# Kernel optimization log

Measured on AMD Instinct MI355X. Metric: run time of the kernel, lower is better.

## Reference

```python
import jax, jax.numpy as jnp
import numpy as np

D_MODEL = 768
NUM_HEADS = 12
HEAD_DIM = D_MODEL // NUM_HEADS  # 64, also rotary dim
INTERMEDIATE = 1152
WINDOW = 128          # config.local_attention (layer_id=1 -> local layer)
ROPE_BASE = 10000.0   # local_rope_theta
EPS = 1e-5


def layer_norm_nocenter(x, gamma):
    # keras LayerNormalization(center=False): mean-subtract, no beta
    mu = jnp.mean(x, axis=-1, keepdims=True)
    var = jnp.var(x, axis=-1, keepdims=True)
    return (x - mu) * jax.lax.rsqrt(var + EPS) * gamma


def rotate_half(x):
    x1, x2 = jnp.split(x, 2, axis=-1)
    return jnp.concatenate([-x2, x1], axis=-1)


def setup_inputs() -> dict:
    key = jax.random.key(0)
    ks = jax.random.split(key, 7)
    B, S = 4, 2048
    hidden_states = jax.random.normal(ks[0], (B, S, D_MODEL), dtype=jnp.float32)
    attention_mask = jnp.zeros((B, 1, S, S), dtype=jnp.float32)  # no padding
    s = 0.02
    attn_norm_gamma = jnp.ones((D_MODEL,), dtype=jnp.float32)
    wqkv = jax.random.normal(ks[1], (D_MODEL, 3 * D_MODEL), dtype=jnp.float32) * s
    wo_attn = jax.random.normal(ks[2], (D_MODEL, D_MODEL), dtype=jnp.float32) * s
    mlp_norm_gamma = jnp.ones((D_MODEL,), dtype=jnp.float32)
    wi = jax.random.normal(ks[3], (D_MODEL, 2 * INTERMEDIATE), dtype=jnp.float32) * s
    wo_mlp = jax.random.normal(ks[4], (INTERMEDIATE, D_MODEL), dtype=jnp.float32) * s
    return {
        'hidden_states': hidden_states,
        'attention_mask': attention_mask,
        'attn_norm_gamma': attn_norm_gamma,
        'wqkv': wqkv,
        'wo_attn': wo_attn,
        'mlp_norm_gamma': mlp_norm_gamma,
        'wi': wi,
        'wo_mlp': wo_mlp,
    }


def reference(hidden_states, attention_mask, attn_norm_gamma, wqkv, wo_attn,
              mlp_norm_gamma, wi, wo_mlp):
    B, S, Dm = hidden_states.shape
    H, Dh = NUM_HEADS, HEAD_DIM

    # RoPE cache (NTKScaling with scaling_factor=1 -> plain RoPE)
    idx = jnp.arange(0, Dh, 2, dtype=jnp.float32)
    inv_freq = 1.0 / (ROPE_BASE ** (idx / Dh))          # [Dh/2]
    t = jnp.arange(S, dtype=jnp.float32)
    freqs = t[:, None] * inv_freq[None, :]              # [S, Dh/2]
    emb = jnp.concatenate([freqs, freqs], axis=-1)      # [S, Dh]
    cos = jnp.cos(emb)[None, None]                      # [1,1,S,Dh]
    sin = jnp.sin(emb)[None, None]

    # combined sliding-window + padding mask
    pos = jnp.arange(S)
    dist = jnp.abs(pos[:, None] - pos[None, :])
    neg = jnp.finfo(jnp.float32).min
    local = jnp.where(dist <= WINDOW // 2, 0.0, neg).astype(jnp.float32)
    mask = attention_mask + local[None, None]           # [B,1,S,S]

    # attention (layer_id != 0 -> pre-norm)
    x = layer_norm_nocenter(hidden_states, attn_norm_gamma)
    qkv = (x @ wqkv).reshape(B, S, 3, H, Dh).transpose(2, 0, 3, 1, 4)
    q, k, v = qkv[0], qkv[1], qkv[2]                    # [B,H,S,Dh]
    q = q * cos + rotate_half(q) * sin
    k = k * cos + rotate_half(k) * sin

    scale = 1.0 / jnp.sqrt(jnp.asarray(Dh, q.dtype))
    scores = jnp.einsum('bhqd,bhkd->bhqk', q, k) * scale + mask
    attn = jax.nn.softmax(scores, axis=-1)
    ctx = jnp.einsum('bhqk,bhkd->bhqd', attn, v)
    attn_out = ctx.transpose(0, 2, 1, 3).reshape(B, S, Dm) @ wo_attn

    h = hidden_states + attn_out

    # GLU MLP: Wi -> split -> gelu(x)*gate -> Wo, residual
    n = layer_norm_nocenter(h, mlp_norm_gamma)
    x_in, gate = jnp.split(n @ wi, 2, axis=-1)
    mlp = jax.nn.gelu(x_in, approximate=False) * gate
    return h + mlp @ wo_mlp
```

## Files before the change

### kernel.cpp

```cpp
#include <hip/hip_runtime.h>
#include <cstdint>
#include <cstddef>

typedef __bf16 bf16;
typedef float f32x4 __attribute__((ext_vector_type(4)));
typedef __bf16 bf16x8 __attribute__((ext_vector_type(8)));
typedef __bf16 bf16x4 __attribute__((ext_vector_type(4)));
typedef __bf16 bf16x2 __attribute__((ext_vector_type(2)));

#define MFMA16(a, b, c) __builtin_amdgcn_mfma_f32_16x16x32_bf16((a), (b), (c), 0, 0, 0)

__device__ __forceinline__ void gload_lds16(const void* g, void* l) {
  __builtin_amdgcn_global_load_lds((__attribute__((address_space(1))) void*)g,
                                   (__attribute__((address_space(3))) void*)l,
                                   16, 0, 0);
}

__global__ __launch_bounds__(256) void wconv_ln(const float* __restrict__ wqkv,
                                                const float* __restrict__ woa,
                                                const float* __restrict__ wi,
                                                const float* __restrict__ wom,
                                                bf16* __restrict__ wqkvT,
                                                bf16* __restrict__ woaT,
                                                bf16* __restrict__ wiT,
                                                bf16* __restrict__ womT,
                                                const float* __restrict__ X,
                                                const float* __restrict__ gamma,
                                                bf16* __restrict__ xnout) {
  __shared__ float tile[32][33];
  const int t = threadIdx.x;
  int id = blockIdx.x;
  if (id >= 4896) {
    const int row = id - 4896;
    const float* xr = X + (size_t)row * 768;
    float v0 = xr[t], v1 = xr[t + 256], v2 = xr[t + 512];
    float s = v0 + v1 + v2;
    float s2 = v0 * v0 + v1 * v1 + v2 * v2;
#pragma unroll
    for (int m = 1; m <= 32; m <<= 1) {
      s += __shfl_xor(s, m, 64);
      s2 += __shfl_xor(s2, m, 64);
    }
    float* red = &tile[0][0];
    const int w = t >> 6, lane = t & 63;
    if (lane == 0) { red[w] = s; red[4 + w] = s2; }
    __syncthreads();
    s = red[0] + red[1] + red[2] + red[3];
    s2 = red[4] + red[5] + red[6] + red[7];
    const float mu = s * (1.f / 768.f);
    const float var = s2 * (1.f / 768.f) - mu * mu;
    const float rs = rsqrtf(var + 1e-5f);
    xnout[(size_t)row * 768 + t] = (bf16)((v0 - mu) * rs * gamma[t]);
    xnout[(size_t)row * 768 + t + 256] = (bf16)((v1 - mu) * rs * gamma[t + 256]);
    xnout[(size_t)row * 768 + t + 512] = (bf16)((v2 - mu) * rs * gamma[t + 512]);
    return;
  }
  const float* W;
  bf16* Wt;
  int K, N, bx, by;
  if (id < 1728) { W = wqkv; Wt = wqkvT; K = 768; N = 2304; bx = id % 72; by = id / 72; }
  else if (id < 2304) { id -= 1728; W = woa; Wt = woaT; K = 768; N = 768; bx = id % 24; by = id / 24; }
  else if (id < 4032) { id -= 2304; W = wi; Wt = wiT; K = 768; N = 2304; bx = id % 72; by = id / 72; }
  else { id -= 4032; W = wom; Wt = womT; K = 1152; N = 768; bx = id % 24; by = id / 24; }
  const int n0 = bx * 32, k0 = by * 32;
  const int c = t & 31, r = t >> 5;
#pragma unroll
  for (int i = 0; i < 4; ++i)
    tile[r + i * 8][c] = W[(size_t)(k0 + r + i * 8) * N + n0 + c];
  __syncthreads();
#pragma unroll
  for (int i = 0; i < 4; ++i)
    Wt[(size_t)(n0 + r + i * 8) * K + k0 + c] = (bf16)tile[c][r + i * 8];
}

__global__ __launch_bounds__(256) void ln_kernel(const float* __restrict__ X,
                                                 const float* __restrict__ gamma,
                                                 bf16* __restrict__ out) {
  const int row = blockIdx.x, t = threadIdx.x;
  const float* xr = X + (size_t)row * 768;
  float v0 = xr[t], v1 = xr[t + 256], v2 = xr[t + 512];
  float s = v0 + v1 + v2;
  float s2 = v0 * v0 + v1 * v1 + v2 * v2;
#pragma unroll
  for (int m = 1; m <= 32; m <<= 1) {
    s += __shfl_xor(s, m, 64);
    s2 += __shfl_xor(s2, m, 64);
  }
  __shared__ float red[8];
  const int w = t >> 6, lane = t & 63;
  if (lane == 0) { red[w] = s; red[4 + w] = s2; }
  __syncthreads();
  s = red[0] + red[1] + red[2] + red[3];
  s2 = red[4] + red[5] + red[6] + red[7];
  const float mu = s * (1.f / 768.f);
  const float var = s2 * (1.f / 768.f) - mu * mu;
  const float rs = rsqrtf(var + 1e-5f);
  out[(size_t)row * 768 + t] = (bf16)((v0 - mu) * rs * gamma[t]);
  out[(size_t)row * 768 + t + 256] = (bf16)((v1 - mu) * rs * gamma[t + 256]);
  out[(size_t)row * 768 + t + 512] = (bf16)((v2 - mu) * rs * gamma[t + 512]);
}

#define GEMM_CORE_LOOP(NT_, AROW_EXPR, BROW_EXPR)                                   \
  auto stage = [&](int tile) {                                                      \
    const int kk0 = tile * 64;                                                      \
    bf16* Ab_ = &SM[(tile & 1) * 24576];                                            \
    bf16* Bb_ = Ab_ + 16384;                                                        \
    _Pragma("unroll") for (int i = 0; i < 4; ++i) {                                 \
      int c = i * 512 + t;                                                          \
      int r = c >> 3, j = (c & 7) ^ (r & 7);                                        \
      gload_lds16(Ap + (size_t)(AROW_EXPR) * Kd + (kk0 + j * 8), &Ab_[c * 8]);      \
    }                                                                               \
    _Pragma("unroll") for (int i = 0; i < 2; ++i) {                                 \
      int c = i * 512 + t;                                                          \
      int r = c >> 3, j = (c & 7) ^ (r & 7);                                        \
      gload_lds16(Bp + (size_t)(BROW_EXPR) * Kd + (kk0 + j * 8), &Bb_[c * 8]);      \
    }                                                                               \
  };                                                                                \
  stage(0);                                                                         \
  stage(1);                                                                         \
  asm volatile("s_waitcnt vmcnt(6)" ::: "memory");                                  \
  __builtin_amdgcn_s_barrier();                                                     \
  __builtin_amdgcn_sched_barrier(0);                                                \
  for (int tt = 0; tt < NT_; ++tt) {                                                \
    const bf16* Ab = &SM[(tt & 1) * 24576];                                         \
    const bf16* Bb = Ab + 16384;                                                    \
    bf16x8 af[4], bfr[4];                                                           \
                                                                \
    _Pragma("unroll") for (int mt = 0; mt < 4; ++mt) {                              \
      int r = wm * 64 + mt * 16 + rm;                                               \
      af[mt] = *(const bf16x8*)&Ab[r * 64 + ((qd ^ (r & 7)) * 8)];                  \
    }                                                                               \
    _Pragma("unroll") for (int nt = 0; nt < 4; ++nt) {                              \
      int r = wn * 64 + nt * 16 + rm;                                               \
      bfr[nt] = *(const bf16x8*)&Bb[r * 64 + ((qd ^ (r & 7)) * 8)];                 \
    }                                                                               \
    __builtin_amdgcn_s_barrier();                                                   \
    __builtin_amdgcn_sched_barrier(0);                                              \
    __builtin_amdgcn_s_setprio(1);                                                  \
    _Pragma("unroll") for (int mt = 0; mt < 4; ++mt)                                \
        _Pragma("unroll") for (int nt = 0; nt < 4; ++nt)                            \
            acc[mt][nt] = MFMA16(af[mt], bfr[nt], acc[mt][nt]);                     \
    __builtin_amdgcn_s_setprio(0);                                                  \
    __builtin_amdgcn_s_barrier();                                                   \
    __builtin_amdgcn_sched_barrier(0);                                              \
                                                                \
    _Pragma("unroll") for (int mt = 0; mt < 4; ++mt) {                              \
      int r = wm * 64 + mt * 16 + rm;                                               \
      af[mt] = *(const bf16x8*)&Ab[r * 64 + (((4 + qd) ^ (r & 7)) * 8)];            \
    }                                                                               \
    _Pragma("unroll") for (int nt = 0; nt < 4; ++nt) {                              \
      int r = wn * 64 + nt * 16 + rm;                                               \
      bfr[nt] = *(const bf16x8*)&Bb[r * 64 + (((4 + qd) ^ (r & 7)) * 8)];           \
    }                                                                               \
    asm volatile("s_waitcnt lgkmcnt(0)" ::: "memory");                              \
    __builtin_amdgcn_sched_barrier(0);                                              \
    __builtin_amdgcn_s_barrier();           \
    __builtin_amdgcn_sched_barrier(0);                                              \
    if (tt + 2 < NT_) stage(tt + 2);                                                \
    __builtin_amdgcn_s_setprio(1);                                                  \
    _Pragma("unroll") for (int mt = 0; mt < 4; ++mt)                                \
        _Pragma("unroll") for (int nt = 0; nt < 4; ++nt)                            \
            acc[mt][nt] = MFMA16(af[mt], bfr[nt], acc[mt][nt]);                     \
    __builtin_amdgcn_s_setprio(0);                                                  \
    if (tt + 2 < NT_) {                                                             \
      asm volatile("s_waitcnt vmcnt(6)" ::: "memory");                              \
    } else {                                                                        \
      asm volatile("s_waitcnt vmcnt(0)" ::: "memory");                              \
    }                                                                               \
    __builtin_amdgcn_s_barrier();                                                   \
    __builtin_amdgcn_sched_barrier(0);                                              \
  }

template <int EPI, int NT>
__global__ __launch_bounds__(512, 2) void gemm_big(const bf16* __restrict__ Ap,
                                                   const bf16* __restrict__ Bp,
                                                   const float* __restrict__ Res,
                                                   void* __restrict__ Cout,
                                                   int Nout) {
  constexpr int Kd = NT * 64;
  __shared__ __align__(16) bf16 SM[49152];
  const int t = threadIdx.x;
  const int lane = t & 63, w = t >> 6;
  const int wm = w >> 1, wn = w & 1;
  const int rm = lane & 15, qd = lane >> 4;
  const int by = blockIdx.y;
  const int row0 = blockIdx.x * 256;
  f32x4 acc[4][4] = {};

  auto brow = [&](int r) -> int {
    if constexpr (EPI == 1) {
      int q = (r >> 4) & 3;
      return ((q & 1) ? 1152 : 0) + by * 64 + (r >> 6) * 32 + ((q >> 1) << 4) + (r & 15);
    } else {
      return by * 128 + r;
    }
  };

  GEMM_CORE_LOOP(NT, row0 + r, brow(r))

  if constexpr (EPI == 0) {
    float* C = (float*)Cout;
#pragma unroll
    for (int mt = 0; mt < 4; ++mt)
#pragma unroll
      for (int nt = 0; nt < 4; ++nt) {
        const int gc = by * 128 + wn * 64 + nt * 16 + rm;
#pragma unroll
        for (int r = 0; r < 4; ++r) {
          const int gr = row0 + wm * 64 + mt * 16 + qd * 4 + r;
          const size_t idx = (size_t)gr * Nout + gc;
          C[idx] = Res[idx] + acc[mt][nt][r];
        }
      }
  } else {
    bf16* C = (bf16*)Cout;
#pragma unroll
    for (int mt = 0; mt < 4; ++mt)
#pragma unroll
      for (int g = 0; g < 2; ++g) {
        const int gc = by * 64 + wn * 32 + g * 16 + rm;
#pragma unroll
        for (int r = 0; r < 4; ++r) {
          const int gr = row0 + wm * 64 + mt * 16 + qd * 4 + r;
          const float x = acc[mt][g * 2][r], gv = acc[mt][g * 2 + 1][r];
          const float ge = 0.5f * x * (1.0f + erff(x * 0.70710678118654752f));
          C[(size_t)gr * 1152 + gc] = (bf16)(ge * gv);
        }
      }
  }
}

__global__ __launch_bounds__(512, 2) void gemm_qkv2(const bf16* __restrict__ Ap,
                                                    const bf16* __restrict__ Bp,
                                                    bf16* __restrict__ Qb,
                                                    bf16* __restrict__ Kb,
                                                    bf16* __restrict__ Vt) {
  constexpr int Kd = 768;
  __shared__ __align__(16) bf16 SM[49152];
  const int t = threadIdx.x;
  const int lane = t & 63, w = t >> 6;
  const int wm = w >> 1, wn = w & 1;
  const int rm = lane & 15, qd = lane >> 4;
  const int by = blockIdx.y;
  const int row0 = blockIdx.x * 256;
  f32x4 acc[4][4] = {};

  GEMM_CORE_LOOP(12, row0 + r, by * 128 + r)

  const int head_id = by * 2 + wn;
  const int typ = by / 6;
  const int b = row0 >> 11;
  const int sblk = row0 & 2047;
  const int sw = sblk + wm * 64;

  if (typ < 2) {
    const int h = head_id - typ * 12;
    const size_t bhbase = (size_t)(b * 12 + h) * 2048;
    bf16* dst = typ ? Kb : Qb;
    constexpr float inv2pi = 0.15915494309189535f;
#pragma unroll
    for (int nt = 0; nt < 2; ++nt) {
      const int d = nt * 16 + rm;
      const float invf = exp2f((float)d * -0.41524101186092029f);
      float rev = (float)(sw + qd * 4) * invf * inv2pi;
      rev -= floorf(rev);
      float cs = __builtin_amdgcn_cosf(rev);
      float sn = __builtin_amdgcn_sinf(rev);
      float rv1 = invf * inv2pi;
      float c1 = __builtin_amdgcn_cosf(rv1), s1 = __builtin_amdgcn_sinf(rv1);
      float rv13 = 13.f * invf * inv2pi;
      rv13 -= floorf(rv13);
      float c13 = __builtin_amdgcn_cosf(rv13), s13 = __builtin_amdgcn_sinf(rv13);
#pragma unroll
      for (int mt = 0; mt < 4; ++mt)
#pragma unroll
        for (int r = 0; r < 4; ++r) {
          const int s = sw + mt * 16 + qd * 4 + r;
          const float x1 = acc[mt][nt][r], x2 = acc[mt][nt + 2][r];
          bf16x2 v2;
          v2[0] = (bf16)(x1 * cs - x2 * sn);
          v2[1] = (bf16)(x2 * cs + x1 * sn);
          *(bf16x2*)&dst[(bhbase + s) * 64 + 2 * d] = v2;
          const float ca = (r < 3) ? c1 : c13, sa = (r < 3) ? s1 : s13;
          const float cn = cs * ca - sn * sa;
          sn = sn * ca + cs * sa;
          cs = cn;
        }
    }
  } else {
#pragma unroll
    for (int mt = 0; mt < 4; ++mt)
#pragma unroll
      for (int nt = 0; nt < 4; ++nt) {
        int hd = wn * 64 + nt * 16 + rm;
        int sl = wm * 64 + mt * 16 + qd * 4;
        bf16x4 v4;
#pragma unroll
        for (int r = 0; r < 4; ++r) v4[r] = (bf16)acc[mt][nt][r];
        *(bf16x4*)&SM[hd * 264 + sl] = v4;
      }
    __syncthreads();
    const int h0 = by * 2 - 24;
#pragma unroll
    for (int it = 0; it < 8; ++it) {
      int cc = it * 512 + t;
      int hd = cc >> 5, s8 = (cc & 31) * 8;
      bf16x8 vv = *(const bf16x8*)&SM[hd * 264 + s8];
      size_t grow = (size_t)(b * 12 + h0 + (hd >> 6)) * 64 + (hd & 63);
      *(bf16x8*)&Vt[grow * 2048 + sblk + s8] = vv;
    }
  }
}

__global__ __launch_bounds__(256) void attn_kernel(const bf16* __restrict__ Qb,
                                                   const bf16* __restrict__ Kb,
                                                   const bf16* __restrict__ Vt,
                                                   const float* __restrict__ am,
                                                   bf16* __restrict__ ctx) {
  __shared__ __align__(16) bf16 KP[64 * 200];
  __shared__ __align__(16) bf16 Vts[64 * 192];
  bf16* Ks = KP;
  bf16* Ps = KP;

  const int t = threadIdx.x;
  const int lane = t & 63, w = t >> 6;
  const int rm = lane & 15, qd = lane >> 4;
  const int s0 = blockIdx.x * 64;
  const int bh = blockIdx.y;
  const int b = bh / 12, h = bh - b * 12;
  const size_t baseQ = (size_t)bh * 2048;

#pragma unroll
  for (int i = 0; i < 6; ++i) {
    int c = i * 256 + t;
    int r = c >> 3, j = (c & 7) ^ (r & 7);
    int key = min(max(s0 - 64 + r, 0), 2047);
    gload_lds16(Kb + (baseQ + key) * 64 + j * 8, &Ks[c * 8]);
  }
#pragma unroll
  for (int i = 0; i < 6; ++i) {
    int c = i * 256 + t;
    int r = c / 24, jl = c - r * 24;
    int j = (jl & 24) | ((jl & 7) ^ (r & 7));
    int k0 = min(max(s0 - 64 + j * 8, 0), 2040);
    gload_lds16(Vt + ((size_t)bh * 64 + r) * 2048 + k0, &Vts[c * 8]);
  }

  bf16x8 aq[2];
#pragma unroll
  for (int kb = 0; kb < 2; ++kb)
    aq[kb] = *(const bf16x8*)&Qb[(baseQ + s0 + w * 16 + rm) * 64 + kb * 32 + qd * 8];

  float msk[12][4];
#pragma unroll
  for (int nt = 0; nt < 12; ++nt) {
    int key = s0 - 64 + nt * 16 + rm;
#pragma unroll
    for (int r = 0; r < 4; ++r) {
      int qpos = s0 + w * 16 + qd * 4 + r;
      bool valid = (key >= 0) && (key < 2048) && (key - qpos <= 64) && (qpos - key <= 64);
      msk[nt][r] = valid ? am[((size_t)b * 2048 + qpos) * 2048 + key] : -3e38f;
    }
  }
  __syncthreads();

  f32x4 sc[12];
#pragma unroll
  for (int nt = 0; nt < 12; ++nt) {
    f32x4 a = {0.f, 0.f, 0.f, 0.f};
#pragma unroll
    for (int kb = 0; kb < 2; ++kb) {
      int r = nt * 16 + rm;
      bf16x8 bk = *(const bf16x8*)&Ks[r * 64 + (((kb * 4 + qd) ^ (rm & 7)) * 8)];
      a = MFMA16(aq[kb], bk, a);
    }
    sc[nt] = a;
  }

  float mx[4] = {-3e38f, -3e38f, -3e38f, -3e38f};
#pragma unroll
  for (int nt = 0; nt < 12; ++nt)
#pragma unroll
    for (int r = 0; r < 4; ++r) {
      float v = (msk[nt][r] <= -2.9e38f) ? -3e38f : sc[nt][r] * 0.125f + msk[nt][r];
      sc[nt][r] = v;
      mx[r] = fmaxf(mx[r], v);
    }
#pragma unroll
  for (int r = 0; r < 4; ++r)
#pragma unroll
    for (int m = 1; m <= 8; m <<= 1) mx[r] = fmaxf(mx[r], __shfl_xor(mx[r], m, 64));
  float sum[4] = {0.f, 0.f, 0.f, 0.f};
#pragma unroll
  for (int nt = 0; nt < 12; ++nt)
#pragma unroll
    for (int r = 0; r < 4; ++r) {
      float p = (sc[nt][r] > -1e37f) ? __expf(sc[nt][r] - mx[r]) : 0.f;
      sc[nt][r] = p;
      sum[r] += p;
    }
#pragma unroll
  for (int r = 0; r < 4; ++r)
#pragma unroll
    for (int m = 1; m <= 8; m <<= 1) sum[r] += __shfl_xor(sum[r], m, 64);
  float inv[4];
#pragma unroll
  for (int r = 0; r < 4; ++r) inv[r] = 1.f / sum[r];

  __syncthreads();

#pragma unroll
  for (int nt = 0; nt < 12; ++nt)
#pragma unroll
    for (int r = 0; r < 4; ++r)
      Ps[(w * 16 + qd * 4 + r) * 200 + nt * 16 + rm] = (bf16)(sc[nt][r] * inv[r]);

  f32x4 o[4] = {};
#pragma unroll
  for (int ks = 0; ks < 6; ++ks) {
    bf16x8 ap = *(const bf16x8*)&Ps[(w * 16 + rm) * 200 + ks * 32 + qd * 8];
#pragma unroll
    for (int nt = 0; nt < 4; ++nt) {
      int kc = ks * 4 + qd;
      bf16x8 bv = *(const bf16x8*)&Vts[(nt * 16 + rm) * 192 +
                                       (((kc & 24) | ((kc & 7) ^ (rm & 7))) * 8)];
      o[nt] = MFMA16(ap, bv, o[nt]);
    }
  }
#pragma unroll
  for (int nt = 0; nt < 4; ++nt)
#pragma unroll
    for (int r = 0; r < 4; ++r) {
      int q_ = s0 + w * 16 + qd * 4 + r;
      ctx[((size_t)(b * 2048 + q_)) * 768 + h * 64 + nt * 16 + rm] = (bf16)o[nt][r];
    }
}

extern "C" void kernel_launch(void* const* d_in, const int* in_sizes, int n_in,
                              void* d_out, int out_size, void* d_ws, size_t ws_size,
                              hipStream_t stream) {
  (void)in_sizes; (void)n_in; (void)out_size; (void)ws_size;
  const float* hidden = (const float*)d_in[0];
  const float* amask = (const float*)d_in[1];
  const float* g1 = (const float*)d_in[2];
  const float* wqkv = (const float*)d_in[3];
  const float* woa = (const float*)d_in[4];
  const float* g2 = (const float*)d_in[5];
  const float* wi = (const float*)d_in[6];
  const float* wom = (const float*)d_in[7];
  float* out = (float*)d_out;

  char* p = (char*)d_ws;
  size_t o = 0;
  auto take = [&](size_t bytes) {
    char* r = p + o;
    o = (o + bytes + 255) & ~(size_t)255;
    return r;
  };
  bf16* wqkvT = (bf16*)take((size_t)2304 * 768 * 2);
  bf16* woaT = (bf16*)take((size_t)768 * 768 * 2);
  bf16* wiT = (bf16*)take((size_t)2304 * 768 * 2);
  bf16* womT = (bf16*)take((size_t)768 * 1152 * 2);
  bf16* xn = (bf16*)take((size_t)8192 * 768 * 2);
  bf16* Qb = (bf16*)take((size_t)98304 * 64 * 2);
  bf16* Kb = (bf16*)take((size_t)98304 * 64 * 2);
  bf16* Vt = (bf16*)take((size_t)98304 * 64 * 2);
  bf16* ctxb = (bf16*)take((size_t)8192 * 768 * 2);
  float* hbuf = (float*)take((size_t)8192 * 768 * 4);
  bf16* mlp = (bf16*)take((size_t)8192 * 1152 * 2);

  wconv_ln<<<13088, 256, 0, stream>>>(wqkv, woa, wi, wom, wqkvT, woaT, wiT, womT,
                                      hidden, g1, xn);

  gemm_qkv2<<<dim3(32, 18), 512, 0, stream>>>(xn, wqkvT, Qb, Kb, Vt);
  attn_kernel<<<dim3(32, 48), 256, 0, stream>>>(Qb, Kb, Vt, amask, ctxb);
  gemm_big<0, 12><<<dim3(32, 6), 512, 0, stream>>>(ctxb, woaT, hidden, hbuf, 768);

  ln_kernel<<<8192, 256, 0, stream>>>(hbuf, g2, xn);
  gemm_big<1, 12><<<dim3(32, 18), 512, 0, stream>>>(xn, wiT, nullptr, mlp, 1152);
  gemm_big<0, 18><<<dim3(32, 6), 512, 0, stream>>>(mlp, womT, hbuf, out, 768);
}
```

Measured before the change: 307.8 us.

## Triple-buffer GEMM LDS tiles and collapse per-k-tile barriers to one

Switches the shared GEMM main loop from double to triple buffering of LDS tiles. The prefetch of tile tt+2 is now issued at the top of each iteration. Both half-k MFMA phases run back-to-back with a single barrier per iteration, replacing the four barriers and the setprio toggling. This is meant to cut barrier stalls and start global loads earlier. LDS per block grows from 96KB to 144KB, so the requested two blocks per CU likely no longer fit in LDS, which halves occupancy.

```diff
diff --git a/kernel.cpp b/kernel.cpp
--- a/kernel.cpp
+++ b/kernel.cpp
@@ -103,7 +103,7 @@
 #define GEMM_CORE_LOOP(NT_, AROW_EXPR, BROW_EXPR)                                   \
   auto stage = [&](int tile) {                                                      \
     const int kk0 = tile * 64;                                                      \
-    bf16* Ab_ = &SM[(tile & 1) * 24576];                                            \
+    bf16* Ab_ = &SM[(tile % 3) * 24576];                                            \
     bf16* Bb_ = Ab_ + 16384;                                                        \
     _Pragma("unroll") for (int i = 0; i < 4; ++i) {                                 \
       int c = i * 512 + t;                                                          \
@@ -122,51 +122,27 @@
   __builtin_amdgcn_s_barrier();                                                     \
   __builtin_amdgcn_sched_barrier(0);                                                \
   for (int tt = 0; tt < NT_; ++tt) {                                                \
-    const bf16* Ab = &SM[(tt & 1) * 24576];                                         \
+    if (tt + 2 < NT_) stage(tt + 2);                                                \
+    const bf16* Ab = &SM[(tt % 3) * 24576];                                         \
     const bf16* Bb = Ab + 16384;                                                    \
     bf16x8 af[4], bfr[4];                                                           \
-                                                                \
-    _Pragma("unroll") for (int mt = 0; mt < 4; ++mt) {                              \
-      int r = wm * 64 + mt * 16 + rm;                                               \
-      af[mt] = *(const bf16x8*)&Ab[r * 64 + ((qd ^ (r & 7)) * 8)];                  \
+    _Pragma("unroll") for (int kb = 0; kb < 2; ++kb) {                              \
+      _Pragma("unroll") for (int mt = 0; mt < 4; ++mt) {                            \
+        int r = wm * 64 + mt * 16 + rm;                                             \
+        af[mt] = *(const bf16x8*)&Ab[r * 64 + (((kb * 4 + qd) ^ (r & 7)) * 8)];     \
+      }                                                                             \
+      _Pragma("unroll") for (int nt = 0; nt < 4; ++nt) {                            \
+        int r = wn * 64 + nt * 16 + rm;                                             \
+        bfr[nt] = *(const bf16x8*)&Bb[r * 64 + (((kb * 4 + qd) ^ (r & 7)) * 8)];    \
+      }                                                                             \
+      _Pragma("unroll") for (int mt = 0; mt < 4; ++mt)                              \
+          _Pragma("unroll") for (int nt = 0; nt < 4; ++nt)                          \
+              acc[mt][nt] = MFMA16(af[mt], bfr[nt], acc[mt][nt]);                   \
     }                                                                               \
-    _Pragma("unroll") for (int nt = 0; nt < 4; ++nt) {                              \
-      int r = wn * 64 + nt * 16 + rm;                                               \
-      bfr[nt] = *(const bf16x8*)&Bb[r * 64 + ((qd ^ (r & 7)) * 8)];                 \
-    }                                                                               \
-    __builtin_amdgcn_s_barrier();                                                   \
     __builtin_amdgcn_sched_barrier(0);                                              \
-    __builtin_amdgcn_s_setprio(1);                                                  \
-    _Pragma("unroll") for (int mt = 0; mt < 4; ++mt)                                \
-        _Pragma("unroll") for (int nt = 0; nt < 4; ++nt)                            \
-            acc[mt][nt] = MFMA16(af[mt], bfr[nt], acc[mt][nt]);                     \
-    __builtin_amdgcn_s_setprio(0);                                                  \
-    __builtin_amdgcn_s_barrier();                                                   \
-    __builtin_amdgcn_sched_barrier(0);                                              \
-                                                                \
-    _Pragma("unroll") for (int mt = 0; mt < 4; ++mt) {                              \
-      int r = wm * 64 + mt * 16 + rm;                                               \
-      af[mt] = *(const bf16x8*)&Ab[r * 64 + (((4 + qd) ^ (r & 7)) * 8)];            \
-    }                                                                               \
-    _Pragma("unroll") for (int nt = 0; nt < 4; ++nt) {                              \
-      int r = wn * 64 + nt * 16 + rm;                                               \
-      bfr[nt] = *(const bf16x8*)&Bb[r * 64 + (((4 + qd) ^ (r & 7)) * 8)];           \
-    }                                                                               \
     asm volatile("s_waitcnt lgkmcnt(0)" ::: "memory");                              \
-    __builtin_amdgcn_sched_barrier(0);                                              \
-    __builtin_amdgcn_s_barrier();           \
-    __builtin_amdgcn_sched_barrier(0);                                              \
-    if (tt + 2 < NT_) stage(tt + 2);                                                \
-    __builtin_amdgcn_s_setprio(1);                                                  \
-    _Pragma("unroll") for (int mt = 0; mt < 4; ++mt)                                \
-        _Pragma("unroll") for (int nt = 0; nt < 4; ++nt)                            \
-            acc[mt][nt] = MFMA16(af[mt], bfr[nt], acc[mt][nt]);                     \
-    __builtin_amdgcn_s_setprio(0);                                                  \
-    if (tt + 2 < NT_) {                                                             \
-      asm volatile("s_waitcnt vmcnt(6)" ::: "memory");                              \
-    } else {                                                                        \
-      asm volatile("s_waitcnt vmcnt(0)" ::: "memory");                              \
-    }                                                                               \
+    if (tt + 2 < NT_) { asm volatile("s_waitcnt vmcnt(6)" ::: "memory"); }          \
+    else if (tt + 1 < NT_) { asm volatile("s_waitcnt vmcnt(0)" ::: "memory"); }     \
     __builtin_amdgcn_s_barrier();                                                   \
     __builtin_amdgcn_sched_barrier(0);                                              \
   }
@@ -178,7 +154,7 @@
                                                    void* __restrict__ Cout,
                                                    int Nout) {
   constexpr int Kd = NT * 64;
-  __shared__ __align__(16) bf16 SM[49152];
+  __shared__ __align__(16) bf16 SM[73728];
   const int t = threadIdx.x;
   const int lane = t & 63, w = t >> 6;
   const int wm = w >> 1, wn = w & 1;
@@ -236,7 +212,7 @@
                                                     bf16* __restrict__ Kb,
                                                     bf16* __restrict__ Vt) {
   constexpr int Kd = 768;
-  __shared__ __align__(16) bf16 SM[49152];
+  __shared__ __align__(16) bf16 SM[73728];
   const int t = threadIdx.x;
   const int lane = t & 63, w = t >> 6;
   const int wm = w >> 1, wn = w & 1;
```

Result: no change. 304.9 us (-0.9%).

## Enlarge GEMM tiles to 256x256 with BK=32 and 4-stage LDS pipeline

Applied to the files above, without the earlier changes.

The shared GEMM core loop now uses 256x256 output tiles per block, with 8 waves laid out 2x4 and 8x4 accumulator fragments per wave. K tiles shrink to 32 with a four-buffer LDS ring, and global-to-LDS loads for the next tile are interleaved between the two MFMA halves. The aim is more reuse per loaded byte and better hiding of load latency. The cost is that grids halve (e.g. 32x3 = 96 blocks for the output projections, below the CU count), accumulator register pressure doubles, and LDS use rises, which can hurt occupancy.

```diff
diff --git a/kernel.cpp b/kernel.cpp
--- a/kernel.cpp
+++ b/kernel.cpp
@@ -101,72 +101,64 @@
 }
 
 #define GEMM_CORE_LOOP(NT_, AROW_EXPR, BROW_EXPR)                                   \
-  auto stage = [&](int tile) {                                                      \
-    const int kk0 = tile * 64;                                                      \
-    bf16* Ab_ = &SM[(tile & 1) * 24576];                                            \
-    bf16* Bb_ = Ab_ + 16384;                                                        \
-    _Pragma("unroll") for (int i = 0; i < 4; ++i) {                                 \
-      int c = i * 512 + t;                                                          \
-      int r = c >> 3, j = (c & 7) ^ (r & 7);                                        \
+  auto stagep = [&](int tile, int p) {                                              \
+    const int kk0 = tile * 32;                                                      \
+    bf16* Ab_ = &SM[(tile & 3) * 16384];                                            \
+    bf16* Bb_ = Ab_ + 8192;                                                         \
+    {                                                                               \
+      int c = p * 512 + t;                                                          \
+      int r = c >> 2, j = (c & 3) ^ (r & 3);                                        \
       gload_lds16(Ap + (size_t)(AROW_EXPR) * Kd + (kk0 + j * 8), &Ab_[c * 8]);      \
     }                                                                               \
-    _Pragma("unroll") for (int i = 0; i < 2; ++i) {                                 \
-      int c = i * 512 + t;                                                          \
-      int r = c >> 3, j = (c & 7) ^ (r & 7);                                        \
+    {                                                                               \
+      int c = p * 512 + t;                                                          \
+      int r = c >> 2, j = (c & 3) ^ (r & 3);                                        \
       gload_lds16(Bp + (size_t)(BROW_EXPR) * Kd + (kk0 + j * 8), &Bb_[c * 8]);      \
     }                                                                               \
   };                                                                                \
-  stage(0);                                                                         \
-  stage(1);                                                                         \
-  asm volatile("s_waitcnt vmcnt(6)" ::: "memory");                                  \
+  stagep(0, 0); stagep(0, 1);                                                       \
+  stagep(1, 0); stagep(1, 1);                                                       \
+  asm volatile("s_waitcnt vmcnt(4)" ::: "memory");                                  \
   __builtin_amdgcn_s_barrier();                                                     \
   __builtin_amdgcn_sched_barrier(0);                                                \
   for (int tt = 0; tt < NT_; ++tt) {                                                \
-    const bf16* Ab = &SM[(tt & 1) * 24576];                                         \
-    const bf16* Bb = Ab + 16384;                                                    \
+    const bf16* Ab = &SM[(tt & 3) * 16384];                                         \
+    const bf16* Bb = Ab + 8192;                                                     \
     bf16x8 af[4], bfr[4];                                                           \
-                                                                \
-    _Pragma("unroll") for (int mt = 0; mt < 4; ++mt) {                              \
-      int r = wm * 64 + mt * 16 + rm;                                               \
-      af[mt] = *(const bf16x8*)&Ab[r * 64 + ((qd ^ (r & 7)) * 8)];                  \
-    }                                                                               \
+                       \
     _Pragma("unroll") for (int nt = 0; nt < 4; ++nt) {                              \
       int r = wn * 64 + nt * 16 + rm;                                               \
-      bfr[nt] = *(const bf16x8*)&Bb[r * 64 + ((qd ^ (r & 7)) * 8)];                 \
+      bfr[nt] = *(const bf16x8*)&Bb[r * 32 + ((qd ^ (r & 3)) * 8)];                 \
     }                                                                               \
+    _Pragma("unroll") for (int mt = 0; mt < 4; ++mt) {                              \
+      int r = wm * 128 + mt * 16 + rm;                                              \
+      af[mt] = *(const bf16x8*)&Ab[r * 32 + ((qd ^ (r & 3)) * 8)];                  \
+    }                                                                               \
+    if (tt + 2 < NT_) stagep(tt + 2, 0);                                            \
     __builtin_amdgcn_s_barrier();                                                   \
     __builtin_amdgcn_sched_barrier(0);                                              \
     __builtin_amdgcn_s_setprio(1);                                                  \
     _Pragma("unroll") for (int mt = 0; mt < 4; ++mt)                                \
-        _Pragma("unroll") for (int nt = 0; nt < 4; ++nt)                            \
-            acc[mt][nt] = MFMA16(af[mt], bfr[nt], acc[mt][nt]);                     \
+      _Pragma("unroll") for (int nt = 0; nt < 4; ++nt)                              \
+        acc[mt][nt] = MFMA16(af[mt], bfr[nt], acc[mt][nt]);                         \
     __builtin_amdgcn_s_setprio(0);                                                  \
     __builtin_amdgcn_s_barrier();                                                   \
     __builtin_amdgcn_sched_barrier(0);                                              \
-                                                                \
+                                                        \
     _Pragma("unroll") for (int mt = 0; mt < 4; ++mt) {                              \
-      int r = wm * 64 + mt * 16 + rm;                                               \
-      af[mt] = *(const bf16x8*)&Ab[r * 64 + (((4 + qd) ^ (r & 7)) * 8)];            \
+      int r = wm * 128 + 64 + mt * 16 + rm;                                         \
+      af[mt] = *(const bf16x8*)&Ab[r * 32 + ((qd ^ (r & 3)) * 8)];                  \
     }                                                                               \
-    _Pragma("unroll") for (int nt = 0; nt < 4; ++nt) {                              \
-      int r = wn * 64 + nt * 16 + rm;                                               \
-      bfr[nt] = *(const bf16x8*)&Bb[r * 64 + (((4 + qd) ^ (r & 7)) * 8)];           \
-    }                                                                               \
-    asm volatile("s_waitcnt lgkmcnt(0)" ::: "memory");                              \
+    if (tt + 2 < NT_) stagep(tt + 2, 1);                                            \
+    __builtin_amdgcn_s_barrier();                                                   \
     __builtin_amdgcn_sched_barrier(0);                                              \
-    __builtin_amdgcn_s_barrier();           \
-    __builtin_amdgcn_sched_barrier(0);                                              \
-    if (tt + 2 < NT_) stage(tt + 2);                                                \
     __builtin_amdgcn_s_setprio(1);                                                  \
     _Pragma("unroll") for (int mt = 0; mt < 4; ++mt)                                \
-        _Pragma("unroll") for (int nt = 0; nt < 4; ++nt)                            \
-            acc[mt][nt] = MFMA16(af[mt], bfr[nt], acc[mt][nt]);                     \
+      _Pragma("unroll") for (int nt = 0; nt < 4; ++nt)                              \
+        acc[4 + mt][nt] = MFMA16(af[mt], bfr[nt], acc[4 + mt][nt]);                 \
     __builtin_amdgcn_s_setprio(0);                                                  \
-    if (tt + 2 < NT_) {                                                             \
-      asm volatile("s_waitcnt vmcnt(6)" ::: "memory");                              \
-    } else {                                                                        \
-      asm volatile("s_waitcnt vmcnt(0)" ::: "memory");                              \
-    }                                                                               \
+    if (tt + 2 < NT_) { asm volatile("s_waitcnt vmcnt(4)" ::: "memory"); }          \
+    else { asm volatile("s_waitcnt vmcnt(0)" ::: "memory"); }                       \
     __builtin_amdgcn_s_barrier();                                                   \
     __builtin_amdgcn_sched_barrier(0);                                              \
   }
@@ -177,22 +169,23 @@
                                                    const float* __restrict__ Res,
                                                    void* __restrict__ Cout,
                                                    int Nout) {
-  constexpr int Kd = NT * 64;
-  __shared__ __align__(16) bf16 SM[49152];
+  constexpr int Kd = NT * 32;
+  __shared__ __align__(16) bf16 SM[65536];
   const int t = threadIdx.x;
   const int lane = t & 63, w = t >> 6;
-  const int wm = w >> 1, wn = w & 1;
+  const int wm = w >> 2, wn = w & 3;
   const int rm = lane & 15, qd = lane >> 4;
   const int by = blockIdx.y;
   const int row0 = blockIdx.x * 256;
-  f32x4 acc[4][4] = {};
+  f32x4 acc[8][4] = {};
 
   auto brow = [&](int r) -> int {
     if constexpr (EPI == 1) {
       int q = (r >> 4) & 3;
-      return ((q & 1) ? 1152 : 0) + by * 64 + (r >> 6) * 32 + ((q >> 1) << 4) + (r & 15);
+      return ((q & 1) ? 1152 : 0) + by * 128 + ((r >> 6) * 32) + (((q >> 1) & 1) * 16) +
+             (r & 15);
     } else {
-      return by * 128 + r;
+      return by * 256 + r;
     }
   };
 
@@ -201,13 +194,13 @@
   if constexpr (EPI == 0) {
     float* C = (float*)Cout;
 #pragma unroll
-    for (int mt = 0; mt < 4; ++mt)
+    for (int mt = 0; mt < 8; ++mt)
 #pragma unroll
       for (int nt = 0; nt < 4; ++nt) {
-        const int gc = by * 128 + wn * 64 + nt * 16 + rm;
+        const int gc = by * 256 + wn * 64 + nt * 16 + rm;
 #pragma unroll
         for (int r = 0; r < 4; ++r) {
-          const int gr = row0 + wm * 64 + mt * 16 + qd * 4 + r;
+          const int gr = row0 + wm * 128 + mt * 16 + qd * 4 + r;
           const size_t idx = (size_t)gr * Nout + gc;
           C[idx] = Res[idx] + acc[mt][nt][r];
         }
@@ -215,13 +208,13 @@
   } else {
     bf16* C = (bf16*)Cout;
 #pragma unroll
-    for (int mt = 0; mt < 4; ++mt)
+    for (int mt = 0; mt < 8; ++mt)
 #pragma unroll
       for (int g = 0; g < 2; ++g) {
-        const int gc = by * 64 + wn * 32 + g * 16 + rm;
+        const int gc = by * 128 + wn * 32 + g * 16 + rm;
 #pragma unroll
         for (int r = 0; r < 4; ++r) {
-          const int gr = row0 + wm * 64 + mt * 16 + qd * 4 + r;
+          const int gr = row0 + wm * 128 + mt * 16 + qd * 4 + r;
           const float x = acc[mt][g * 2][r], gv = acc[mt][g * 2 + 1][r];
           const float ge = 0.5f * x * (1.0f + erff(x * 0.70710678118654752f));
           C[(size_t)gr * 1152 + gc] = (bf16)(ge * gv);
@@ -236,25 +229,24 @@
                                                     bf16* __restrict__ Kb,
                                                     bf16* __restrict__ Vt) {
   constexpr int Kd = 768;
-  __shared__ __align__(16) bf16 SM[49152];
+  __shared__ __align__(16) bf16 SM[69632];
   const int t = threadIdx.x;
   const int lane = t & 63, w = t >> 6;
-  const int wm = w >> 1, wn = w & 1;
+  const int wm = w >> 2, wn = w & 3;
   const int rm = lane & 15, qd = lane >> 4;
   const int by = blockIdx.y;
   const int row0 = blockIdx.x * 256;
-  f32x4 acc[4][4] = {};
-
-  GEMM_CORE_LOOP(12, row0 + r, by * 128 + r)
-
-  const int head_id = by * 2 + wn;
-  const int typ = by / 6;
+  f32x4 acc[8][4] = {};
+
+  GEMM_CORE_LOOP(24, row0 + r, by * 256 + r)
+
+  const int typ = by / 3;
   const int b = row0 >> 11;
   const int sblk = row0 & 2047;
-  const int sw = sblk + wm * 64;
+  const int sw = sblk + wm * 128;
 
   if (typ < 2) {
-    const int h = head_id - typ * 12;
+    const int h = (by % 3) * 4 + wn;
     const size_t bhbase = (size_t)(b * 12 + h) * 2048;
     bf16* dst = typ ? Kb : Qb;
     constexpr float inv2pi = 0.15915494309189535f;
@@ -272,7 +264,7 @@
       rv13 -= floorf(rv13);
       float c13 = __builtin_amdgcn_cosf(rv13), s13 = __builtin_amdgcn_sinf(rv13);
 #pragma unroll
-      for (int mt = 0; mt < 4; ++mt)
+      for (int mt = 0; mt < 8; ++mt)
 #pragma unroll
         for (int r = 0; r < 4; ++r) {
           const int s = sw + mt * 16 + qd * 4 + r;
@@ -289,20 +281,20 @@
     }
   } else {
 #pragma unroll
-    for (int mt = 0; mt < 4; ++mt)
+    for (int mt = 0; mt < 8; ++mt)
 #pragma unroll
       for (int nt = 0; nt < 4; ++nt) {
         int hd = wn * 64 + nt * 16 + rm;
-        int sl = wm * 64 + mt * 16 + qd * 4;
+        int sl = wm * 128 + mt * 16 + qd * 4;
         bf16x4 v4;
 #pragma unroll
         for (int r = 0; r < 4; ++r) v4[r] = (bf16)acc[mt][nt][r];
         *(bf16x4*)&SM[hd * 264 + sl] = v4;
       }
     __syncthreads();
-    const int h0 = by * 2 - 24;
-#pragma unroll
-    for (int it = 0; it < 8; ++it) {
+    const int h0 = (by - 6) * 4;
+#pragma unroll
+    for (int it = 0; it < 16; ++it) {
       int cc = it * 512 + t;
       int hd = cc >> 5, s8 = (cc & 31) * 8;
       bf16x8 vv = *(const bf16x8*)&SM[hd * 264 + s8];
@@ -472,11 +464,11 @@
   wconv_ln<<<13088, 256, 0, stream>>>(wqkv, woa, wi, wom, wqkvT, woaT, wiT, womT,
                                       hidden, g1, xn);
 
-  gemm_qkv2<<<dim3(32, 18), 512, 0, stream>>>(xn, wqkvT, Qb, Kb, Vt);
+  gemm_qkv2<<<dim3(32, 9), 512, 0, stream>>>(xn, wqkvT, Qb, Kb, Vt);
   attn_kernel<<<dim3(32, 48), 256, 0, stream>>>(Qb, Kb, Vt, amask, ctxb);
-  gemm_big<0, 12><<<dim3(32, 6), 512, 0, stream>>>(ctxb, woaT, hidden, hbuf, 768);
+  gemm_big<0, 24><<<dim3(32, 3), 512, 0, stream>>>(ctxb, woaT, hidden, hbuf, 768);
 
   ln_kernel<<<8192, 256, 0, stream>>>(hbuf, g2, xn);
-  gemm_big<1, 12><<<dim3(32, 18), 512, 0, stream>>>(xn, wiT, nullptr, mlp, 1152);
-  gemm_big<0, 18><<<dim3(32, 6), 512, 0, stream>>>(mlp, womT, hbuf, out, 768);
-}
+  gemm_big<1, 24><<<dim3(32, 9), 512, 0, stream>>>(xn, wiT, nullptr, mlp, 1152);
+  gemm_big<0, 36><<<dim3(32, 3), 512, 0, stream>>>(mlp, womT, hbuf, out, 768);
+}
```

Measured after the change: 359.2 us. 1.17x slower.

## Replace double-buffered 256-row GEMMs with single-buffered 128x128 tile kernels

Applied to the files above, without the earlier changes.

Swaps the QKV projection and the two N=768 output GEMMs (attention out-proj and MLP down-proj) from the 512-thread, 256-row, double-buffered GEMM core to simpler 256-thread kernels with 128x128 tiles and a single LDS buffer. The grid doubles along M, giving more blocks for the N=768 GEMMs (384 instead of 192) to fill the CUs. The cost is that the global-to-LDS prefetch no longer overlaps with MFMA work, and there is less reuse per tile. The fused RoPE and V-transpose epilogue is kept, with its smaller LDS staging layout.

```diff
diff --git a/kernel.cpp b/kernel.cpp
--- a/kernel.cpp
+++ b/kernel.cpp
@@ -100,6 +100,184 @@
   out[(size_t)row * 768 + t + 512] = (bf16)((v2 - mu) * rs * gamma[t + 512]);
 }
 
+template <int BM, bool RES, typename TOUT>
+__global__ __launch_bounds__(256) void gemm_bt(const bf16* __restrict__ A,
+                                               const bf16* __restrict__ Bt,
+                                               const float* __restrict__ Res,
+                                               TOUT* __restrict__ C, int M, int N, int K) {
+  constexpr int MT = BM / 32;
+  __shared__ __align__(16) bf16 As[BM * 64];
+  __shared__ __align__(16) bf16 Bs[128 * 64];
+  const int t = threadIdx.x;
+  const int lane = t & 63;
+  const int w = t >> 6;
+  const int wm = w >> 1, wn = w & 1;
+  const int row0 = blockIdx.x * BM, col0 = blockIdx.y * 128;
+  const int rm = lane & 15, qd = lane >> 4;
+  f32x4 acc[MT][4] = {};
+  for (int k0 = 0; k0 < K; k0 += 64) {
+#pragma unroll
+    for (int i = 0; i < BM / 32; ++i) {
+      int c = i * 256 + t;
+      int r = c >> 3, j = (c & 7) ^ (r & 7);
+      gload_lds16(A + (size_t)(row0 + r) * K + (k0 + j * 8), &As[c * 8]);
+    }
+#pragma unroll
+    for (int i = 0; i < 4; ++i) {
+      int c = i * 256 + t;
+      int r = c >> 3, j = (c & 7) ^ (r & 7);
+      gload_lds16(Bt + (size_t)(col0 + r) * K + (k0 + j * 8), &Bs[c * 8]);
+    }
+    __syncthreads();
+#pragma unroll
+    for (int kb = 0; kb < 2; ++kb) {
+      bf16x8 af[MT], bfr[4];
+#pragma unroll
+      for (int mt = 0; mt < MT; ++mt) {
+        int r = wm * (MT * 16) + mt * 16 + rm;
+        af[mt] = *(const bf16x8*)&As[r * 64 + (((kb * 4 + qd) ^ (r & 7)) * 8)];
+      }
+#pragma unroll
+      for (int nt = 0; nt < 4; ++nt) {
+        int r = wn * 64 + nt * 16 + rm;
+        bfr[nt] = *(const bf16x8*)&Bs[r * 64 + (((kb * 4 + qd) ^ (r & 7)) * 8)];
+      }
+#pragma unroll
+      for (int mt = 0; mt < MT; ++mt)
+#pragma unroll
+        for (int nt = 0; nt < 4; ++nt)
+          acc[mt][nt] = MFMA16(af[mt], bfr[nt], acc[mt][nt]);
+    }
+    __syncthreads();
+  }
+#pragma unroll
+  for (int mt = 0; mt < MT; ++mt)
+#pragma unroll
+    for (int nt = 0; nt < 4; ++nt) {
+      const int gc = col0 + wn * 64 + nt * 16 + rm;
+#pragma unroll
+      for (int r = 0; r < 4; ++r) {
+        const int gr = row0 + wm * (MT * 16) + mt * 16 + qd * 4 + r;
+        float v = acc[mt][nt][r];
+        const size_t idx = (size_t)gr * N + gc;
+        if (RES) v += Res[idx];
+        C[idx] = (TOUT)v;
+      }
+    }
+}
+
+__global__ __launch_bounds__(256) void gemm_qkv(const bf16* __restrict__ A,
+                                                const bf16* __restrict__ Bt,
+                                                bf16* __restrict__ Qb,
+                                                bf16* __restrict__ Kb,
+                                                bf16* __restrict__ Vt) {
+  __shared__ __align__(16) bf16 SM[17408];
+  bf16* As = SM;
+  bf16* Bs = SM + 8192;
+
+  const int t = threadIdx.x;
+  const int lane = t & 63;
+  const int w = t >> 6;
+  const int wm = w >> 1, wn = w & 1;
+  const int row0 = blockIdx.x * 128, col0 = blockIdx.y * 128;
+  const int rm = lane & 15, qd = lane >> 4;
+  f32x4 acc[4][4] = {};
+  for (int k0 = 0; k0 < 768; k0 += 64) {
+#pragma unroll
+    for (int i = 0; i < 4; ++i) {
+      int c = i * 256 + t;
+      int r = c >> 3, j = (c & 7) ^ (r & 7);
+      gload_lds16(A + (size_t)(row0 + r) * 768 + (k0 + j * 8), &As[c * 8]);
+      gload_lds16(Bt + (size_t)(col0 + r) * 768 + (k0 + j * 8), &Bs[c * 8]);
+    }
+    __syncthreads();
+#pragma unroll
+    for (int kb = 0; kb < 2; ++kb) {
+      bf16x8 af[4], bfr[4];
+#pragma unroll
+      for (int mt = 0; mt < 4; ++mt) {
+        int r = wm * 64 + mt * 16 + rm;
+        af[mt] = *(const bf16x8*)&As[r * 64 + (((kb * 4 + qd) ^ (r & 7)) * 8)];
+      }
+#pragma unroll
+      for (int nt = 0; nt < 4; ++nt) {
+        int r = wn * 64 + nt * 16 + rm;
+        bfr[nt] = *(const bf16x8*)&Bs[r * 64 + (((kb * 4 + qd) ^ (r & 7)) * 8)];
+      }
+#pragma unroll
+      for (int mt = 0; mt < 4; ++mt)
+#pragma unroll
+        for (int nt = 0; nt < 4; ++nt)
+          acc[mt][nt] = MFMA16(af[mt], bfr[nt], acc[mt][nt]);
+    }
+    __syncthreads();
+  }
+
+  const int head_id = blockIdx.y * 2 + wn;
+  const int typ = blockIdx.y / 6;
+  const int b = row0 >> 11;
+  const int sblk = row0 & 2047;
+  const int sw = sblk + wm * 64;
+
+  if (typ < 2) {
+    const int h = head_id - typ * 12;
+    const size_t bhbase = (size_t)(b * 12 + h) * 2048;
+    bf16* dst = typ ? Kb : Qb;
+    constexpr float inv2pi = 0.15915494309189535f;
+#pragma unroll
+    for (int nt = 0; nt < 2; ++nt) {
+      const int d = nt * 16 + rm;
+      const float invf = exp2f((float)d * -0.41524101186092029f);
+      float rev = (float)(sw + qd * 4) * invf * inv2pi;
+      rev -= floorf(rev);
+      float cs = __builtin_amdgcn_cosf(rev);
+      float sn = __builtin_amdgcn_sinf(rev);
+      float rv1 = invf * inv2pi;
+      float c1 = __builtin_amdgcn_cosf(rv1), s1 = __builtin_amdgcn_sinf(rv1);
+      float rv13 = 13.f * invf * inv2pi;
+      rv13 -= floorf(rv13);
+      float c13 = __builtin_amdgcn_cosf(rv13), s13 = __builtin_amdgcn_sinf(rv13);
+#pragma unroll
+      for (int mt = 0; mt < 4; ++mt)
+#pragma unroll
+        for (int r = 0; r < 4; ++r) {
+          const int s = sw + mt * 16 + qd * 4 + r;
+          const float x1 = acc[mt][nt][r], x2 = acc[mt][nt + 2][r];
+          bf16x2 v2;
+          v2[0] = (bf16)(x1 * cs - x2 * sn);
+          v2[1] = (bf16)(x2 * cs + x1 * sn);
+          *(bf16x2*)&dst[(bhbase + s) * 64 + 2 * d] = v2;
+          const float ca = (r < 3) ? c1 : c13, sa = (r < 3) ? s1 : s13;
+          const float cn = cs * ca - sn * sa;
+          sn = sn * ca + cs * sa;
+          cs = cn;
+        }
+    }
+  } else {
+#pragma unroll
+    for (int mt = 0; mt < 4; ++mt)
+#pragma unroll
+      for (int nt = 0; nt < 4; ++nt) {
+        int hd = wn * 64 + nt * 16 + rm;
+        int sl = wm * 64 + mt * 16 + qd * 4;
+        bf16x4 v4;
+#pragma unroll
+        for (int r = 0; r < 4; ++r) v4[r] = (bf16)acc[mt][nt][r];
+        *(bf16x4*)&SM[hd * 136 + sl] = v4;
+      }
+    __syncthreads();
+    const int h0 = blockIdx.y * 2 - 24;
+#pragma unroll
+    for (int it = 0; it < 8; ++it) {
+      int cc = it * 256 + t;
+      int hd = cc >> 4, s8 = (cc & 15) * 8;
+      bf16x8 vv = *(const bf16x8*)&SM[hd * 136 + s8];
+      size_t grow = (size_t)(b * 12 + h0 + (hd >> 6)) * 64 + (hd & 63);
+      *(bf16x8*)&Vt[grow * 2048 + sblk + s8] = vv;
+    }
+  }
+}
+
 #define GEMM_CORE_LOOP(NT_, AROW_EXPR, BROW_EXPR)                                   \
   auto stage = [&](int tile) {                                                      \
     const int kk0 = tile * 64;                                                      \
@@ -227,88 +405,6 @@
           C[(size_t)gr * 1152 + gc] = (bf16)(ge * gv);
         }
       }
-  }
-}
-
-__global__ __launch_bounds__(512, 2) void gemm_qkv2(const bf16* __restrict__ Ap,
-                                                    const bf16* __restrict__ Bp,
-                                                    bf16* __restrict__ Qb,
-                                                    bf16* __restrict__ Kb,
-                                                    bf16* __restrict__ Vt) {
-  constexpr int Kd = 768;
-  __shared__ __align__(16) bf16 SM[49152];
-  const int t = threadIdx.x;
-  const int lane = t & 63, w = t >> 6;
-  const int wm = w >> 1, wn = w & 1;
-  const int rm = lane & 15, qd = lane >> 4;
-  const int by = blockIdx.y;
-  const int row0 = blockIdx.x * 256;
-  f32x4 acc[4][4] = {};
-
-  GEMM_CORE_LOOP(12, row0 + r, by * 128 + r)
-
-  const int head_id = by * 2 + wn;
-  const int typ = by / 6;
-  const int b = row0 >> 11;
-  const int sblk = row0 & 2047;
-  const int sw = sblk + wm * 64;
-
-  if (typ < 2) {
-    const int h = head_id - typ * 12;
-    const size_t bhbase = (size_t)(b * 12 + h) * 2048;
-    bf16* dst = typ ? Kb : Qb;
-    constexpr float inv2pi = 0.15915494309189535f;
-#pragma unroll
-    for (int nt = 0; nt < 2; ++nt) {
-      const int d = nt * 16 + rm;
-      const float invf = exp2f((float)d * -0.41524101186092029f);
-      float rev = (float)(sw + qd * 4) * invf * inv2pi;
-      rev -= floorf(rev);
-      float cs = __builtin_amdgcn_cosf(rev);
-      float sn = __builtin_amdgcn_sinf(rev);
-      float rv1 = invf * inv2pi;
-      float c1 = __builtin_amdgcn_cosf(rv1), s1 = __builtin_amdgcn_sinf(rv1);
-      float rv13 = 13.f * invf * inv2pi;
-      rv13 -= floorf(rv13);
-      float c13 = __builtin_amdgcn_cosf(rv13), s13 = __builtin_amdgcn_sinf(rv13);
-#pragma unroll
-      for (int mt = 0; mt < 4; ++mt)
-#pragma unroll
-        for (int r = 0; r < 4; ++r) {
-          const int s = sw + mt * 16 + qd * 4 + r;
-          const float x1 = acc[mt][nt][r], x2 = acc[mt][nt + 2][r];
-          bf16x2 v2;
-          v2[0] = (bf16)(x1 * cs - x2 * sn);
-          v2[1] = (bf16)(x2 * cs + x1 * sn);
-          *(bf16x2*)&dst[(bhbase + s) * 64 + 2 * d] = v2;
-          const float ca = (r < 3) ? c1 : c13, sa = (r < 3) ? s1 : s13;
-          const float cn = cs * ca - sn * sa;
-          sn = sn * ca + cs * sa;
-          cs = cn;
-        }
-    }
-  } else {
-#pragma unroll
-    for (int mt = 0; mt < 4; ++mt)
-#pragma unroll
-      for (int nt = 0; nt < 4; ++nt) {
-        int hd = wn * 64 + nt * 16 + rm;
-        int sl = wm * 64 + mt * 16 + qd * 4;
-        bf16x4 v4;
-#pragma unroll
-        for (int r = 0; r < 4; ++r) v4[r] = (bf16)acc[mt][nt][r];
-        *(bf16x4*)&SM[hd * 264 + sl] = v4;
-      }
-    __syncthreads();
-    const int h0 = by * 2 - 24;
-#pragma unroll
-    for (int it = 0; it < 8; ++it) {
-      int cc = it * 512 + t;
-      int hd = cc >> 5, s8 = (cc & 31) * 8;
-      bf16x8 vv = *(const bf16x8*)&SM[hd * 264 + s8];
-      size_t grow = (size_t)(b * 12 + h0 + (hd >> 6)) * 64 + (hd & 63);
-      *(bf16x8*)&Vt[grow * 2048 + sblk + s8] = vv;
-    }
   }
 }
 
@@ -472,11 +568,13 @@
   wconv_ln<<<13088, 256, 0, stream>>>(wqkv, woa, wi, wom, wqkvT, woaT, wiT, womT,
                                       hidden, g1, xn);
 
-  gemm_qkv2<<<dim3(32, 18), 512, 0, stream>>>(xn, wqkvT, Qb, Kb, Vt);
+  gemm_qkv<<<dim3(64, 18), 256, 0, stream>>>(xn, wqkvT, Qb, Kb, Vt);
   attn_kernel<<<dim3(32, 48), 256, 0, stream>>>(Qb, Kb, Vt, amask, ctxb);
-  gemm_big<0, 12><<<dim3(32, 6), 512, 0, stream>>>(ctxb, woaT, hidden, hbuf, 768);
+  gemm_bt<128, true, float><<<dim3(64, 6), 256, 0, stream>>>(ctxb, woaT, hidden, hbuf,
+                                                             8192, 768, 768);
 
   ln_kernel<<<8192, 256, 0, stream>>>(hbuf, g2, xn);
   gemm_big<1, 12><<<dim3(32, 18), 512, 0, stream>>>(xn, wiT, nullptr, mlp, 1152);
-  gemm_big<0, 18><<<dim3(32, 6), 512, 0, stream>>>(mlp, womT, hbuf, out, 768);
-}
+  gemm_bt<128, true, float><<<dim3(64, 6), 256, 0, stream>>>(mlp, womT, hbuf, out,
+                                                             8192, 768, 1152);
+}
```

Measured after the change: 318.9 us. 1.04x slower.
